# Kernel tuning notes

Measured on AMD Instinct MI355X. Metric: run time of the kernel, lower is better.

Reference implementation:

```python
import jax, jax.numpy as jnp
import numpy as np
from jax import lax

T, B, IN, H = 26246, 128, 6, 1  # seq_len, batch, input_size, hidden_size(=output_size)

def setup_inputs() -> dict:
    key = jax.random.key(0)
    ks = jax.random.split(key, 7)
    return {
        "x": jax.random.normal(ks[0], (T, B, IN), dtype=jnp.float32),
        "W_ih": jax.random.normal(ks[1], (H, IN), dtype=jnp.float32) * 0.3,
        "W_hh": jax.random.normal(ks[2], (H, H), dtype=jnp.float32) * 0.3,
        "b_ih": jax.random.normal(ks[3], (H,), dtype=jnp.float32) * 0.1,
        "b_hh": jax.random.normal(ks[4], (H,), dtype=jnp.float32) * 0.1,
        "fc_w": jax.random.normal(ks[5], (H, H), dtype=jnp.float32),
        "fc_b": jax.random.normal(ks[6], (H,), dtype=jnp.float32) * 0.1,
    }

def reference(x, W_ih, W_hh, b_ih, b_hh, fc_w, fc_b):
    # Vanilla tanh RNN (nn.RNN, batch_first=False): h_t = tanh(x_t W_ih^T + b_ih + h_{t-1} W_hh^T + b_hh)
    # Precompute the input projection for all timesteps in one GEMM: [T,B,H]
    xp = jnp.einsum('tbi,hi->tbh', x, W_ih) + b_ih + b_hh

    def step(h, xt):  # h: [B,H], xt: [B,H]
        h_new = jnp.tanh(xt + h @ W_hh.T)
        return h_new, h_new

    h0 = jnp.zeros((B, H), dtype=x.dtype)
    _, hs = lax.scan(step, h0, xp)      # hs: [T,B,H] — full output sequence
    # Trailing Linear applied per timestep
    out = hs @ fc_w.T + fc_b            # [T,B,H]
    return out
```

## Files before the change

kernel.cpp:

```cpp
#include <hip/hip_runtime.h>
#include <math.h>

#define T_LEN 26246
#define B_SZ  128
#define SCALE 2.88539008177792681472f

#define CHUNK 56
#define UNR   8
#define NCH   ((T_LEN + CHUNK - 1) / CHUNK)

__global__ __launch_bounds__(128) void rnn_scan_fused(
    const float* __restrict__ x, const float* __restrict__ W_ih,
    const float* __restrict__ W_hh, const float* __restrict__ b_ih,
    const float* __restrict__ b_hh, const float* __restrict__ fc_w,
    const float* __restrict__ fc_b, float* __restrict__ out) {
  const int b  = threadIdx.x;
  const int c  = blockIdx.x;
  const int t0 = c * CHUNK;

  const float w  = W_hh[0];
  const float w2 = SCALE * w;
  const float s0 = SCALE * W_ih[0], s1 = SCALE * W_ih[1], s2 = SCALE * W_ih[2],
              s3 = SCALE * W_ih[3], s4 = SCALE * W_ih[4], s5 = SCALE * W_ih[5];
  const float sb = SCALE * (b_ih[0] + b_hh[0]);
  const float fw = fc_w[0], fb = fc_b[0];

  int warm = 16;
  {
    float aw = fabsf(w);
    if (aw > 0.56f) {
      float l = logf(fminf(aw, 0.999f));
      warm = (int)ceilf(-9.2103404f / l);
      warm = (warm + UNR - 1) & ~(UNR - 1);
      if (warm > 2048) warm = 2048;
    }
  }
  int tw = t0 - warm;
  if (tw < 0) tw = 0;
  const int tlim = t0 + CHUNK;

  float h = 0.0f;
  float2 buf[UNR][3], nbuf[UNR][3];

  #pragma unroll
  for (int j = 0; j < UNR; ++j) {
    int t = tw + j; t = (t < T_LEN) ? t : (T_LEN - 1);
    const float2* p = (const float2*)(x + ((size_t)t * B_SZ + b) * 6);
    buf[j][0] = p[0]; buf[j][1] = p[1]; buf[j][2] = p[2];
  }

  for (int tb = tw; tb < tlim; tb += UNR) {
    #pragma unroll
    for (int j = 0; j < UNR; ++j) {
      int t = tb + UNR + j; t = (t < T_LEN) ? t : (T_LEN - 1);
      const float2* p = (const float2*)(x + ((size_t)t * B_SZ + b) * 6);
      nbuf[j][0] = p[0]; nbuf[j][1] = p[1]; nbuf[j][2] = p[2];
    }
    #pragma unroll
    for (int j = 0; j < UNR; ++j) {
      float a = fmaf(buf[j][0].x, s0, sb);
      a = fmaf(buf[j][0].y, s1, a);
      a = fmaf(buf[j][1].x, s2, a);
      a = fmaf(buf[j][1].y, s3, a);
      a = fmaf(buf[j][2].x, s4, a);
      a = fmaf(buf[j][2].y, s5, a);
      float g = fmaf(h, w2, a);
      float u = __builtin_amdgcn_exp2f(g);
      float r = __builtin_amdgcn_rcpf(u + 1.0f);
      h = fmaf(-2.0f, r, 1.0f);
      const int t = tb + j;
      if (t >= t0 && t < T_LEN) out[(size_t)t * B_SZ + b] = fmaf(h, fw, fb);
    }
    #pragma unroll
    for (int j = 0; j < UNR; ++j) {
      buf[j][0] = nbuf[j][0]; buf[j][1] = nbuf[j][1]; buf[j][2] = nbuf[j][2];
    }
  }
}

extern "C" void kernel_launch(void* const* d_in, const int* in_sizes, int n_in,
                              void* d_out, int out_size, void* d_ws, size_t ws_size,
                              hipStream_t stream) {
  const float* x    = (const float*)d_in[0];
  const float* W_ih = (const float*)d_in[1];
  const float* W_hh = (const float*)d_in[2];
  const float* b_ih = (const float*)d_in[3];
  const float* b_hh = (const float*)d_in[4];
  const float* fc_w = (const float*)d_in[5];
  const float* fc_b = (const float*)d_in[6];
  float* out = (float*)d_out;

  rnn_scan_fused<<<NCH, 128, 0, stream>>>(x, W_ih, W_hh, b_ih, b_hh,
                                          fc_w, fc_b, out);
}
```

Baseline: 24.53 us.

## Stage input projection through LDS with coalesced float4 loads per time group

Each thread now loads a contiguous 48-float slab of x (eight timesteps' worth for one batch-slot position) as float4s, computes eight projections and writes them to a double-buffered LDS array. Each thread then reads its own batch column's projected values back for the serial tanh recurrence. The projection work and x loads move off the per-step critical path, and global reads become fully coalesced 16-byte accesses. In exchange it adds LDS traffic, a __syncthreads per group and a changed chunk size, and it removes the rounding of the warmup length to a multiple of the group size.

```diff
diff --git a/kernel.cpp b/kernel.cpp
--- a/kernel.cpp
+++ b/kernel.cpp
@@ -5,9 +5,14 @@
 #define B_SZ  128
 #define SCALE 2.88539008177792681472f
 
-#define CHUNK 56
-#define UNR   8
+#define CHUNK 52
+#define G     8
 #define NCH   ((T_LEN + CHUNK - 1) / CHUNK)
+#define TOTAL_F4 ((size_t)T_LEN * 192)
+
+#define XF(n) (((n) & 3) == 0 ? xr[(n) >> 2].x : \
+               ((n) & 3) == 1 ? xr[(n) >> 2].y : \
+               ((n) & 3) == 2 ? xr[(n) >> 2].z : xr[(n) >> 2].w)
 
 __global__ __launch_bounds__(128) void rnn_scan_fused(
     const float* __restrict__ x, const float* __restrict__ W_ih,
@@ -15,8 +20,10 @@
     const float* __restrict__ b_hh, const float* __restrict__ fc_w,
     const float* __restrict__ fc_b, float* __restrict__ out) {
   const int b  = threadIdx.x;
-  const int c  = blockIdx.x;
-  const int t0 = c * CHUNK;
+  const int k  = threadIdx.x;
+  const int t0 = blockIdx.x * CHUNK;
+
+  __shared__ float a_lds[2][G * B_SZ];
 
   const float w  = W_hh[0];
   const float w2 = SCALE * w;
@@ -31,50 +38,73 @@
     if (aw > 0.56f) {
       float l = logf(fminf(aw, 0.999f));
       warm = (int)ceilf(-9.2103404f / l);
-      warm = (warm + UNR - 1) & ~(UNR - 1);
       if (warm > 2048) warm = 2048;
     }
   }
   int tw = t0 - warm;
   if (tw < 0) tw = 0;
-  const int tlim = t0 + CHUNK;
+  const int steps   = t0 + CHUNK - tw;
+  const int ngroups = (steps + G - 1) / G;
+
+  float4 xr[12];
+
+  auto LOADX = [&](int tg) {
+    size_t base = (size_t)tg * 192 + 12 * (size_t)k;
+    #pragma unroll
+    for (int i = 0; i < 12; ++i) {
+      size_t idx = base + i;
+      if (idx >= TOTAL_F4) idx = TOTAL_F4 - 1;
+      xr[i] = ((const float4*)x)[idx];
+    }
+  };
+
+  auto PROJ = [&](int cur) {
+    float av[G];
+    #pragma unroll
+    for (int e = 0; e < G; ++e) {
+      float a = fmaf(XF(6 * e + 0), s0, sb);
+      a = fmaf(XF(6 * e + 1), s1, a);
+      a = fmaf(XF(6 * e + 2), s2, a);
+      a = fmaf(XF(6 * e + 3), s3, a);
+      a = fmaf(XF(6 * e + 4), s4, a);
+      a = fmaf(XF(6 * e + 5), s5, a);
+      av[e] = a;
+    }
+    float4* dst = (float4*)&a_lds[cur][8 * k];
+    dst[0] = make_float4(av[0], av[1], av[2], av[3]);
+    dst[1] = make_float4(av[4], av[5], av[6], av[7]);
+  };
+
+  LOADX(tw);
+  PROJ(0);
+  LOADX(tw + G);
+  __syncthreads();
 
   float h = 0.0f;
-  float2 buf[UNR][3], nbuf[UNR][3];
+  int cur = 0;
+  for (int g = 0; g < ngroups; ++g) {
+    float areg[G];
+    #pragma unroll
+    for (int j = 0; j < G; ++j) areg[j] = a_lds[cur][j * B_SZ + b];
 
-  #pragma unroll
-  for (int j = 0; j < UNR; ++j) {
-    int t = tw + j; t = (t < T_LEN) ? t : (T_LEN - 1);
-    const float2* p = (const float2*)(x + ((size_t)t * B_SZ + b) * 6);
-    buf[j][0] = p[0]; buf[j][1] = p[1]; buf[j][2] = p[2];
-  }
+    if (g + 1 < ngroups) {
+      PROJ(cur ^ 1);
+      LOADX(tw + G * (g + 2));
+    }
 
-  for (int tb = tw; tb < tlim; tb += UNR) {
+    const int tg = tw + G * g;
     #pragma unroll
-    for (int j = 0; j < UNR; ++j) {
-      int t = tb + UNR + j; t = (t < T_LEN) ? t : (T_LEN - 1);
-      const float2* p = (const float2*)(x + ((size_t)t * B_SZ + b) * 6);
-      nbuf[j][0] = p[0]; nbuf[j][1] = p[1]; nbuf[j][2] = p[2];
+    for (int j = 0; j < G; ++j) {
+      float gz = fmaf(h, w2, areg[j]);
+      float u  = __builtin_amdgcn_exp2f(gz);
+      float r  = __builtin_amdgcn_rcpf(u + 1.0f);
+      h = fmaf(-2.0f, r, 1.0f);
+      const int t = tg + j;
+      if (t >= t0 && t < t0 + CHUNK && t < T_LEN)
+        out[(size_t)t * B_SZ + b] = fmaf(h, fw, fb);
     }
-    #pragma unroll
-    for (int j = 0; j < UNR; ++j) {
-      float a = fmaf(buf[j][0].x, s0, sb);
-      a = fmaf(buf[j][0].y, s1, a);
-      a = fmaf(buf[j][1].x, s2, a);
-      a = fmaf(buf[j][1].y, s3, a);
-      a = fmaf(buf[j][2].x, s4, a);
-      a = fmaf(buf[j][2].y, s5, a);
-      float g = fmaf(h, w2, a);
-      float u = __builtin_amdgcn_exp2f(g);
-      float r = __builtin_amdgcn_rcpf(u + 1.0f);
-      h = fmaf(-2.0f, r, 1.0f);
-      const int t = tb + j;
-      if (t >= t0 && t < T_LEN) out[(size_t)t * B_SZ + b] = fmaf(h, fw, fb);
-    }
-    #pragma unroll
-    for (int j = 0; j < UNR; ++j) {
-      buf[j][0] = nbuf[j][0]; buf[j][1] = nbuf[j][1]; buf[j][2] = nbuf[j][2];
-    }
+    __syncthreads();
+    cur ^= 1;
   }
 }
 
```

Measured after the change: 26.25 us. +7.0%, slower.
